# Performance work log

Measured on AMD Instinct MI355X. Metric: run time of the kernel, lower is better.

## Reference

```python
import jax, jax.numpy as jnp
import numpy as np

STRIDE = 8  # model.fpn.out_strides[level_i=0]


def setup_inputs() -> dict:
    key = jax.random.key(0)
    k1, k2, k3, k4 = jax.random.split(key, 4)
    nB, nA, nH, nW, nC = 16, 3, 128, 128, 80
    t_xywha = jax.random.normal(k1, (nB, nA, nH, nW, 5), dtype=jnp.float32)
    conf_logits = jax.random.normal(k2, (nB, nA, nH, nW, 1), dtype=jnp.float32)
    cls_logits = jax.random.normal(k3, (nB, nA, nH, nW, nC), dtype=jnp.float32)
    # anchors for this FPN level (indices [0,1,2]); positive w/h in pixels
    anchors = jax.random.uniform(k4, (nA, 2), dtype=jnp.float32, minval=16.0, maxval=256.0)
    return {"t_xywha": t_xywha, "conf_logits": conf_logits,
            "cls_logits": cls_logits, "anchors": anchors}


def reference(t_xywha, conf_logits, cls_logits, anchors):
    nB, nA, nH, nW, _ = t_xywha.shape
    # angle: pred_range == 360, loss name 'period_L1' (not LL1/LL2)
    p_radian = jax.nn.sigmoid(t_xywha[..., 4]) * (2.0 * jnp.pi) - jnp.pi
    y_ = jnp.arange(nH, dtype=t_xywha.dtype)
    x_ = jnp.arange(nW, dtype=t_xywha.dtype)
    mesh_y, mesh_x = jnp.meshgrid(y_, x_, indexing="ij")  # [nH, nW]
    px = (jax.nn.sigmoid(t_xywha[..., 0]) + mesh_x) * STRIDE
    py = (jax.nn.sigmoid(t_xywha[..., 1]) + mesh_y) * STRIDE
    pwh = jnp.exp(t_xywha[..., 2:4]) * anchors.reshape(1, nA, 1, 1, 2)
    pdeg = p_radian / jnp.pi * 180.0
    p_xywha = jnp.concatenate(
        [px[..., None], py[..., None], pwh, pdeg[..., None]], axis=-1
    ).reshape(nB, nA * nH * nW, 5)

    p_conf = jax.nn.sigmoid(conf_logits)                # [nB,nA,nH,nW,1]
    p_cls = jax.nn.sigmoid(cls_logits)                  # [nB,nA,nH,nW,nC]
    cls_score = jnp.max(p_cls, axis=-1, keepdims=True)  # [nB,nA,nH,nW,1]
    cls_idx = jnp.argmax(p_cls, axis=-1)                # [nB,nA,nH,nW]
    confs = (p_conf * cls_score).reshape(nB, nA * nH * nW)
    return p_xywha, cls_idx.reshape(nB, nA * nH * nW), confs
```

## Files before the change

### kernel.cpp

```cpp
#include <hip/hip_runtime.h>
#include <math.h>

constexpr int nB = 16, nA = 3, nH = 128, nW = 128, nC = 80;
constexpr int HW   = nH * nW;
constexpr int NPOS = nB * nA * HW;

__device__ __forceinline__ float sigmoidf_fast(float x) {
    return 1.0f / (1.0f + __expf(-x));
}

__global__ __launch_bounds__(256) void yolo_decode_kernel(
    const float* __restrict__ t_xywha,
    const float* __restrict__ conf,
    const float* __restrict__ cls,
    const float* __restrict__ anchors,
    float* __restrict__ out)
{
    const int hw = blockIdx.x * 256 + threadIdx.x;
    const int ba = blockIdx.y;
    const int a  = ba % nA;
    const int h  = hw >> 7;
    const int w  = hw & 127;

    const long long p = (long long)ba * HW + hw;

    const float4* __restrict__ c4 = (const float4*)(cls + p * nC);
    float m = -INFINITY;
    int idx = 0;
#pragma unroll
    for (int i = 0; i < nC / 4; ++i) {
        float4 v = c4[i];
        if (v.x > m) { m = v.x; idx = 4 * i + 0; }
        if (v.y > m) { m = v.y; idx = 4 * i + 1; }
        if (v.z > m) { m = v.z; idx = 4 * i + 2; }
        if (v.w > m) { m = v.w; idx = 4 * i + 3; }
    }

    const float* tp = t_xywha + p * 5;
    const float tx = tp[0], ty = tp[1], tw = tp[2], th = tp[3], ta = tp[4];

    const float aw = anchors[a * 2 + 0];
    const float ah = anchors[a * 2 + 1];

    const float px   = (sigmoidf_fast(tx) + (float)w) * 8.0f;
    const float py   = (sigmoidf_fast(ty) + (float)h) * 8.0f;
    const float pw   = __expf(tw) * aw;
    const float ph   = __expf(th) * ah;
    const float pdeg = sigmoidf_fast(ta) * 360.0f - 180.0f;

    const float cf = sigmoidf_fast(conf[p]) * sigmoidf_fast(m);

    float* op = out + p * 5;
    op[0] = px; op[1] = py; op[2] = pw; op[3] = ph; op[4] = pdeg;

    out[(long long)NPOS * 5 + p] = (float)idx;
    out[(long long)NPOS * 6 + p] = cf;
}

extern "C" void kernel_launch(void* const* d_in, const int* in_sizes, int n_in,
                              void* d_out, int out_size, void* d_ws, size_t ws_size,
                              hipStream_t stream) {
    const float* t_xywha = (const float*)d_in[0];
    const float* conf    = (const float*)d_in[1];
    const float* cls     = (const float*)d_in[2];
    const float* anchors = (const float*)d_in[3];
    float* out = (float*)d_out;

    dim3 grid(HW / 256, nB * nA);
    dim3 block(256);
    yolo_decode_kernel<<<grid, block, 0, stream>>>(t_xywha, conf, cls, anchors, out);
}
```

Before: 370.3 us.

## Cooperative 4-lane class argmax per position for coalesced cls loads

Each group of 4 lanes now reads one position's 80 class logits with interleaved float4 loads, instead of one thread streaming its own 320-byte row. Partial max/argmax results are merged with xor shuffles, with ties broken toward the lower index, and then redistributed to the owning thread. Each wave processes 16 positions per pass over 4 passes. This is meant to turn strided per-thread loads into coalesced ones, at the cost of extra shuffle work.

```diff
diff --git a/kernel.cpp b/kernel.cpp
--- a/kernel.cpp
+++ b/kernel.cpp
@@ -2,8 +2,8 @@
 #include <math.h>
 
 constexpr int nB = 16, nA = 3, nH = 128, nW = 128, nC = 80;
-constexpr int HW   = nH * nW;
-constexpr int NPOS = nB * nA * HW;
+constexpr int HW = nH * nW;
+constexpr long long NPOS = (long long)nB * nA * HW;
 
 __device__ __forceinline__ float sigmoidf_fast(float x) {
     return 1.0f / (1.0f + __expf(-x));
@@ -16,27 +16,53 @@
     const float* __restrict__ anchors,
     float* __restrict__ out)
 {
-    const int hw = blockIdx.x * 256 + threadIdx.x;
+    const int tid  = threadIdx.x;
+    const int lane = tid & 63;
+    const int hwBlock = blockIdx.x * 256;
     const int ba = blockIdx.y;
     const int a  = ba % nA;
-    const int h  = hw >> 7;
-    const int w  = hw & 127;
 
-    const long long p = (long long)ba * HW + hw;
+    const long long blockPos = (long long)ba * HW + hwBlock;
+    const long long wavePos  = blockPos + (tid & ~63);
 
-    const float4* __restrict__ c4 = (const float4*)(cls + p * nC);
-    float m = -INFINITY;
-    int idx = 0;
-#pragma unroll
-    for (int i = 0; i < nC / 4; ++i) {
-        float4 v = c4[i];
-        if (v.x > m) { m = v.x; idx = 4 * i + 0; }
-        if (v.y > m) { m = v.y; idx = 4 * i + 1; }
-        if (v.z > m) { m = v.z; idx = 4 * i + 2; }
-        if (v.w > m) { m = v.w; idx = 4 * i + 3; }
+    const int g = lane >> 2;
+    const int j = lane & 3;
+    const int myPass    = lane >> 4;
+    const int mySrcLane = (lane & 15) << 2;
+
+    float myM = -INFINITY; int myIdx = 0;
+
+    #pragma unroll
+    for (int k = 0; k < 4; ++k) {
+        const long long p = wavePos + k * 16 + g;
+        const float4* __restrict__ c4 = (const float4*)(cls + p * nC);
+        float m = -INFINITY; int idx = 0;
+        #pragma unroll
+        for (int i = 0; i < 5; ++i) {
+            const float4 v = c4[j + 4 * i];
+            const int base = 4 * (j + 4 * i);
+            if (v.x > m) { m = v.x; idx = base + 0; }
+            if (v.y > m) { m = v.y; idx = base + 1; }
+            if (v.z > m) { m = v.z; idx = base + 2; }
+            if (v.w > m) { m = v.w; idx = base + 3; }
+        }
+        #pragma unroll
+        for (int d = 1; d <= 2; d <<= 1) {
+            const float om = __shfl_xor(m, d);
+            const int   oi = __shfl_xor(idx, d);
+            if (om > m || (om == m && oi < idx)) { m = om; idx = oi; }
+        }
+        const float rm = __shfl(m, mySrcLane);
+        const int   ri = __shfl(idx, mySrcLane);
+        if (myPass == k) { myM = rm; myIdx = ri; }
     }
 
-    const float* tp = t_xywha + p * 5;
+    const long long q = blockPos + tid;
+    const int hw = hwBlock + tid;
+    const int h = hw >> 7;
+    const int w = hw & 127;
+
+    const float* tp = t_xywha + q * 5;
     const float tx = tp[0], ty = tp[1], tw = tp[2], th = tp[3], ta = tp[4];
 
     const float aw = anchors[a * 2 + 0];
@@ -48,13 +74,13 @@
     const float ph   = __expf(th) * ah;
     const float pdeg = sigmoidf_fast(ta) * 360.0f - 180.0f;
 
-    const float cf = sigmoidf_fast(conf[p]) * sigmoidf_fast(m);
+    const float cf = sigmoidf_fast(conf[q]) * sigmoidf_fast(myM);
 
-    float* op = out + p * 5;
+    float* op = out + q * 5;
     op[0] = px; op[1] = py; op[2] = pw; op[3] = ph; op[4] = pdeg;
 
-    out[(long long)NPOS * 5 + p] = (float)idx;
-    out[(long long)NPOS * 6 + p] = cf;
+    out[NPOS * 5 + q] = (float)myIdx;
+    out[NPOS * 6 + q] = cf;
 }
 
 extern "C" void kernel_launch(void* const* d_in, const int* in_sizes, int n_in,
```

New measurement: 360.4 us. -2.7%, faster.

## Coalesce class-logit and box loads via shared-memory staged partial argmax

Applied to the files above, without the earlier changes.

Each block of 128 threads now reads its positions' class logits as contiguous float4s across the whole block, so consecutive threads touch consecutive addresses instead of each thread walking its own 320-byte row. Each thread computes a per-float4 partial max and index into padded shared memory, then after a barrier each thread reduces the 20 partials for its own position. The 5-float box inputs and outputs are also staged through shared memory so that global reads and writes are coalesced. The cost is extra shared memory, two barriers and a smaller block size, which may lower occupancy.

```diff
diff --git a/kernel.cpp b/kernel.cpp
--- a/kernel.cpp
+++ b/kernel.cpp
@@ -2,59 +2,85 @@
 #include <math.h>
 
 constexpr int nB = 16, nA = 3, nH = 128, nW = 128, nC = 80;
-constexpr int HW   = nH * nW;
+constexpr int HW = nH * nW;
 constexpr int NPOS = nB * nA * HW;
+constexpr int TPB = 128;
+constexpr int SEG = 20;
+constexpr int PAD = 21;
 
 __device__ __forceinline__ float sigmoidf_fast(float x) {
     return 1.0f / (1.0f + __expf(-x));
 }
 
-__global__ __launch_bounds__(256) void yolo_decode_kernel(
+__global__ __launch_bounds__(TPB) void yolo_decode_kernel(
     const float* __restrict__ t_xywha,
     const float* __restrict__ conf,
     const float* __restrict__ cls,
     const float* __restrict__ anchors,
     float* __restrict__ out)
 {
-    const int hw = blockIdx.x * 256 + threadIdx.x;
-    const int ba = blockIdx.y;
-    const int a  = ba % nA;
-    const int h  = hw >> 7;
-    const int w  = hw & 127;
+    __shared__ float pm[TPB * PAD];
+    __shared__ int   pi[TPB * PAD];
+    __shared__ float txy[TPB * 5];
 
-    const long long p = (long long)ba * HW + hw;
+    const int t    = threadIdx.x;
+    const int base = blockIdx.x * TPB;
 
-    const float4* __restrict__ c4 = (const float4*)(cls + p * nC);
-    float m = -INFINITY;
-    int idx = 0;
-#pragma unroll
-    for (int i = 0; i < nC / 4; ++i) {
-        float4 v = c4[i];
-        if (v.x > m) { m = v.x; idx = 4 * i + 0; }
-        if (v.y > m) { m = v.y; idx = 4 * i + 1; }
-        if (v.z > m) { m = v.z; idx = 4 * i + 2; }
-        if (v.w > m) { m = v.w; idx = 4 * i + 3; }
+    const float4* __restrict__ c4 = (const float4*)(cls + (long long)base * nC);
+    int p = t / 20, s = t % 20;
+    #pragma unroll
+    for (int i = 0; i < SEG; ++i) {
+        const float4 v = c4[t + TPB * i];
+        float m = v.x; int id = 4 * s;
+        if (v.y > m) { m = v.y; id = 4 * s + 1; }
+        if (v.z > m) { m = v.z; id = 4 * s + 2; }
+        if (v.w > m) { m = v.w; id = 4 * s + 3; }
+        pm[p * PAD + s] = m;
+        pi[p * PAD + s] = id;
+        p += 6; s += 8; if (s >= 20) { s -= 20; p += 1; }
     }
 
-    const float* tp = t_xywha + p * 5;
-    const float tx = tp[0], ty = tp[1], tw = tp[2], th = tp[3], ta = tp[4];
+    const float* __restrict__ txyg = t_xywha + (long long)base * 5;
+    #pragma unroll
+    for (int i = 0; i < 5; ++i) txy[t + TPB * i] = txyg[t + TPB * i];
 
-    const float aw = anchors[a * 2 + 0];
-    const float ah = anchors[a * 2 + 1];
+    __syncthreads();
+
+    float m = -INFINITY; int idx = 0;
+    #pragma unroll
+    for (int s2 = 0; s2 < SEG; ++s2) {
+        const float v = pm[t * PAD + s2];
+        if (v > m) { m = v; idx = pi[t * PAD + s2]; }
+    }
+
+    const int q = base + t;
+    const int w = q & 127;
+    const int h = (q >> 7) & 127;
+    const int a = (q >> 14) % 3;
+
+    const float tx = txy[5 * t + 0], ty = txy[5 * t + 1];
+    const float tw = txy[5 * t + 2], th = txy[5 * t + 3];
+    const float ta = txy[5 * t + 4];
+    const float aw = anchors[2 * a + 0];
+    const float ah = anchors[2 * a + 1];
 
     const float px   = (sigmoidf_fast(tx) + (float)w) * 8.0f;
     const float py   = (sigmoidf_fast(ty) + (float)h) * 8.0f;
     const float pw   = __expf(tw) * aw;
     const float ph   = __expf(th) * ah;
     const float pdeg = sigmoidf_fast(ta) * 360.0f - 180.0f;
+    const float cf   = sigmoidf_fast(conf[q]) * sigmoidf_fast(m);
 
-    const float cf = sigmoidf_fast(conf[p]) * sigmoidf_fast(m);
+    out[NPOS * 5 + q] = (float)idx;
+    out[NPOS * 6 + q] = cf;
 
-    float* op = out + p * 5;
-    op[0] = px; op[1] = py; op[2] = pw; op[3] = ph; op[4] = pdeg;
+    txy[5 * t + 0] = px; txy[5 * t + 1] = py; txy[5 * t + 2] = pw;
+    txy[5 * t + 3] = ph; txy[5 * t + 4] = pdeg;
+    __syncthreads();
 
-    out[(long long)NPOS * 5 + p] = (float)idx;
-    out[(long long)NPOS * 6 + p] = cf;
+    float* __restrict__ og = out + (long long)base * 5;
+    #pragma unroll
+    for (int i = 0; i < 5; ++i) og[t + TPB * i] = txy[t + TPB * i];
 }
 
 extern "C" void kernel_launch(void* const* d_in, const int* in_sizes, int n_in,
@@ -66,7 +92,7 @@
     const float* anchors = (const float*)d_in[3];
     float* out = (float*)d_out;
 
-    dim3 grid(HW / 256, nB * nA);
-    dim3 block(256);
+    dim3 grid(NPOS / TPB);
+    dim3 block(TPB);
     yolo_decode_kernel<<<grid, block, 0, stream>>>(t_xywha, conf, cls, anchors, out);
 }
```

Result: faster. 358.3 us (-3.3%).
